# Performance work log

Hardware: AMD Instinct MI355X
Metric: run time of the kernel (lower is better)

The kernel has to match this reference:

```python
import jax, jax.numpy as jnp
import numpy as np


def _conv2d(x, w, b, stride, pad):
    out = jax.lax.conv_general_dilated(
        x, w, (stride, stride), [(pad, pad), (pad, pad)],
        dimension_numbers=('NCHW', 'OIHW', 'NCHW'))
    return out + b[None, :, None, None]


def setup_inputs() -> dict:
    key = jax.random.key(0)
    ks = jax.random.split(key, 7)
    B, C, H, W = 8, 64, 128, 128
    OC, KH, KW = 64, 3, 3
    K = KH * KW
    stdv = 1.0 / np.sqrt(C * KH * KW)
    x = jax.random.normal(ks[0], (B, C, H, W), dtype=jnp.float32)
    weight = jax.random.uniform(ks[1], (OC, C, KH, KW), minval=-stdv, maxval=stdv, dtype=jnp.float32)
    bias = jnp.zeros((OC,), dtype=jnp.float32)
    # original inits these to zero (degenerate); use small random values so the
    # learned-offset bilinear sampling path is actually exercised
    offset_w = jax.random.normal(ks[2], (2 * K, C, KH, KW), dtype=jnp.float32) * 0.01
    offset_b = jax.random.normal(ks[3], (2 * K,), dtype=jnp.float32) * 0.1
    mask_w = jax.random.normal(ks[4], (K, C, KH, KW), dtype=jnp.float32) * 0.01
    mask_b = jax.random.normal(ks[5], (K,), dtype=jnp.float32) * 0.1
    return {"x": x, "weight": weight, "bias": bias,
            "offset_w": offset_w, "offset_b": offset_b,
            "mask_w": mask_w, "mask_b": mask_b}


def _deform_conv2d(x, weight, bias, offset, mask, stride, pad):
    B, C, H, W = x.shape
    OC, _, KH, KW = weight.shape
    K = KH * KW
    Ho, Wo = offset.shape[2], offset.shape[3]
    # offset channel layout: [dy_0, dx_0, dy_1, dx_1, ...] (torchvision)
    off = offset.reshape(B, K, 2, Ho, Wo)
    dy, dx = off[:, :, 0], off[:, :, 1]            # [B,K,Ho,Wo]
    ky, kx = jnp.meshgrid(jnp.arange(KH), jnp.arange(KW), indexing='ij')
    ky = ky.reshape(1, K, 1, 1).astype(x.dtype)
    kx = kx.reshape(1, K, 1, 1).astype(x.dtype)
    gy = (jnp.arange(Ho) * stride - pad).astype(x.dtype)[None, None, :, None]
    gx = (jnp.arange(Wo) * stride - pad).astype(x.dtype)[None, None, None, :]
    py = gy + ky + dy                              # [B,K,Ho,Wo] sample rows
    px = gx + kx + dx                              # [B,K,Ho,Wo] sample cols

    y0 = jnp.floor(py); x0 = jnp.floor(px)
    fy = py - y0; fx = px - x0
    y0i = y0.astype(jnp.int32); x0i = x0.astype(jnp.int32)

    x_flat = x.reshape(B, C, H * W)
    gather = jax.vmap(lambda xf, ix: jnp.take(xf, ix, axis=1))  # -> [B,C,K,Ho,Wo]

    val = jnp.zeros((B, C, K, Ho, Wo), dtype=x.dtype)
    corners = [(y0i, x0i, (1 - fy) * (1 - fx)),
               (y0i, x0i + 1, (1 - fy) * fx),
               (y0i + 1, x0i, fy * (1 - fx)),
               (y0i + 1, x0i + 1, fy * fx)]
    for yy, xx, wt in corners:
        valid = ((yy >= 0) & (yy < H) & (xx >= 0) & (xx < W)).astype(x.dtype)
        idx = jnp.clip(yy, 0, H - 1) * W + jnp.clip(xx, 0, W - 1)
        val = val + (wt * valid)[:, None] * gather(x_flat, idx)

    sampled = val * mask[:, None]                  # modulated (DCNv2)
    w_r = weight.reshape(OC, C, K)
    out = jnp.einsum('bckhw,ock->bohw', sampled, w_r)
    return out + bias[None, :, None, None]


def reference(x, weight, bias, offset_w, offset_b, mask_w, mask_b):
    stride, pad = 1, 1
    offset = _conv2d(x, offset_w, offset_b, stride, pad)
    mask = jax.nn.sigmoid(_conv2d(x, mask_w, mask_b, stride, pad))
    return _deform_conv2d(x, weight, bias, offset, mask, stride, pad)
```

## Files before the change

kernel.cpp:

```cpp
#include <hip/hip_runtime.h>

#define HH 128
#define WW 128
#define CC 64
#define OCC 64
#define BB 8
#define NPIX (BB * HH * WW)

typedef __attribute__((ext_vector_type(4))) float f32x4;
typedef __attribute__((ext_vector_type(2))) float f32x2;
typedef __attribute__((ext_vector_type(8))) short bf16x8;
typedef __attribute__((ext_vector_type(4))) unsigned u32x4;

#define XT_OFF 0
#define W1F_OFF 16777216
#define W2F_OFF 16814080
#define WS_FULL (16814080 + 73728)

#define WROWS 4
#define WCOLS 68
#define WIN_BYTES (WROWS * WCOLS * 128)
#define WLDS_FLOATS (64 * 72)

__device__ __forceinline__ short f2bf(float f) {
    union { float f; unsigned u; } v; v.f = f;
    unsigned r = v.u + 0x7FFF + ((v.u >> 16) & 1);
    return (short)(r >> 16);
}

__device__ __forceinline__ unsigned cvtpk_bf16(float lo, float hi) {
    unsigned r;
    asm("v_cvt_pk_bf16_f32 %0, %1, %2" : "=v"(r) : "v"(lo), "v"(hi));
    return r;
}

__device__ __forceinline__ bf16x8 bilerp8(bf16x8 r00, bf16x8 r01, bf16x8 r10, bf16x8 r11,
                                          f32x4 w) {
    u32x4 u00 = __builtin_bit_cast(u32x4, r00);
    u32x4 u01 = __builtin_bit_cast(u32x4, r01);
    u32x4 u10 = __builtin_bit_cast(u32x4, r10);
    u32x4 u11 = __builtin_bit_cast(u32x4, r11);
    u32x4 res;
#pragma unroll
    for (int j = 0; j < 4; j++) {
        f32x2 a, acc;
        a[0] = __builtin_bit_cast(float, (unsigned)(u00[j] << 16));
        a[1] = __builtin_bit_cast(float, (unsigned)(u00[j] & 0xFFFF0000u));
        acc = a * w[0];
        a[0] = __builtin_bit_cast(float, (unsigned)(u01[j] << 16));
        a[1] = __builtin_bit_cast(float, (unsigned)(u01[j] & 0xFFFF0000u));
        acc += a * w[1];
        a[0] = __builtin_bit_cast(float, (unsigned)(u10[j] << 16));
        a[1] = __builtin_bit_cast(float, (unsigned)(u10[j] & 0xFFFF0000u));
        acc += a * w[2];
        a[0] = __builtin_bit_cast(float, (unsigned)(u11[j] << 16));
        a[1] = __builtin_bit_cast(float, (unsigned)(u11[j] & 0xFFFF0000u));
        acc += a * w[3];
        res[j] = cvtpk_bf16(acc[0], acc[1]);
    }
    return __builtin_bit_cast(bf16x8, res);
}

__global__ void prep_weights(const float* __restrict__ weight,
                             const float* __restrict__ offset_w,
                             const float* __restrict__ mask_w,
                             short* __restrict__ w1f, short* __restrict__ w2f) {
    int tid = blockIdx.x * 256 + threadIdx.x;
    if (tid < 2 * 18 * 64 * 8) {
        int i = tid & 7, lane = (tid >> 3) & 63, ch = (tid >> 9) % 18, tile = tid / (18 * 512);
        int r = tile * 16 + (lane & 15);
        int q = ch * 32 + ((lane >> 4) << 3) + i;
        int k = q >> 6, c = q & 63;
        float v = 0.f;
        if (r < 18)      v = offset_w[(r * CC + c) * 9 + k];
        else if (r < 27) v = mask_w[((r - 18) * CC + c) * 9 + k];
        w1f[tid] = f2bf(v);
    } else {
        int u = tid - 18432;
        if (u < 4 * 18 * 64 * 8) {
            int i = u & 7, lane = (u >> 3) & 63, ch = (u >> 9) % 18, tile = u / (18 * 512);
            int oc = tile * 16 + (lane & 15);
            int q = ch * 32 + ((lane >> 4) << 3) + i;
            int k = q >> 6, c = q & 63;
            w2f[u] = f2bf(weight[(oc * CC + c) * 9 + k]);
        }
    }
}

__global__ __launch_bounds__(256) void transpose_x(
    const float* __restrict__ x, unsigned short* __restrict__ xt) {
    __shared__ float lds[128 * 65];
    int bh = blockIdx.x;
    int b = bh >> 7, h = bh & 127;
    const float* xr = x + ((size_t)b * CC * HH + h) * WW;
    int tid = threadIdx.x;
#pragma unroll
    for (int it = 0; it < 32; it++) {
        int e = it * 256 + tid;
        int c = e >> 7, w = e & 127;
        lds[w * 65 + c] = xr[(size_t)c * HH * WW + w];
    }
    __syncthreads();
    unsigned* otr = (unsigned*)(xt + (size_t)bh * WW * CC);
#pragma unroll
    for (int it = 0; it < 16; it++) {
        int e = it * 256 + tid;
        int w = e >> 5, cp = e & 31;
        unsigned lo = (unsigned short)f2bf(lds[w * 65 + 2 * cp]);
        unsigned hi = (unsigned short)f2bf(lds[w * 65 + 2 * cp + 1]);
        otr[e] = lo | (hi << 16);
    }
}

__global__ __launch_bounds__(256) void fused_mfma(
    const unsigned short* __restrict__ xt,
    const float* __restrict__ offset_b,
    const float* __restrict__ mask_b,
    const float* __restrict__ bias,
    const short* __restrict__ w1f,
    const short* __restrict__ w2f,
    float* __restrict__ out) {
    __shared__ char shbuf[WIN_BYTES + WLDS_FLOATS * 4];
    char* win = shbuf;
    float* wlds = (float*)(shbuf + WIN_BYTES);
    float* colds = wlds;

    int lane = threadIdx.x & 63;
    int wv = threadIdx.x >> 6;
    int bid = blockIdx.x;
    int logical = (bid & 7) * 256 + (bid >> 3);
    int col = lane & 15;
    int qg = lane >> 4;
    int pl = wv * 16 + col;
    int p = logical * 64 + pl;
    int ow = p & (WW - 1);
    int oh = (p >> 7) & (HH - 1);
    int b = p >> 14;
    int ow0 = ow & ~63;
    const unsigned short* xb = xt + (size_t)b * CC * HH * WW;

    int ylo = max(0, oh - 1), yhi = min(HH - 1, oh + 2);
    int xlo = max(0, ow0 - 2), xhi = min(WW - 1, ow0 + 65);
    int R = yhi - ylo + 1, C = xhi - xlo + 1;

    {
        int C8 = C * 8;
        for (int ry = 0; ry < R; ry++) {
            const unsigned short* src = xb + ((size_t)(ylo + ry) * WW + xlo) * CC;
            for (int t = threadIdx.x; t < C8; t += 256) {
                int rx = t >> 3, s = t & 7;
                u32x4 v = *(const u32x4*)(src + rx * CC + s * 8);
                int pix = ry * WCOLS + rx;
                *(u32x4*)(win + (pix << 7) + ((s ^ (pix & 7)) << 4)) = v;
            }
        }
    }
    __syncthreads();

    {
        f32x4 acc0 = {0.f,0.f,0.f,0.f}, acc1 = {0.f,0.f,0.f,0.f};
#pragma unroll
        for (int ch = 0; ch < 18; ch++) {
            int k = ch >> 1;
            int iy = oh - 1 + k / 3;
            int ix = ow - 1 + (k - (k / 3) * 3);
            bool vv = (iy >= 0) && (iy < HH) && (ix >= 0) && (ix < WW);
            bf16x8 bfr = {0,0,0,0,0,0,0,0};
            if (vv) {
                int pix = (iy - ylo) * WCOLS + (ix - xlo);
                int s = ((ch & 1) << 2) + qg;
                bfr = *(const bf16x8*)(win + (pix << 7) + ((s ^ (pix & 7)) << 4));
            }
            bf16x8 a0 = *(const bf16x8*)(w1f + ((size_t)(0 * 18 + ch) * 64 + lane) * 8);
            bf16x8 a1 = *(const bf16x8*)(w1f + ((size_t)(1 * 18 + ch) * 64 + lane) * 8);
            acc0 = __builtin_amdgcn_mfma_f32_16x16x32_bf16(a0, bfr, acc0, 0, 0, 0);
            acc1 = __builtin_amdgcn_mfma_f32_16x16x32_bf16(a1, bfr, acc1, 0, 0, 0);
        }
#pragma unroll
        for (int j = 0; j < 4; j++) {
            int r0 = (qg << 2) + j;
            int r1 = 16 + r0;
            float b1 = (r1 < 18) ? offset_b[r1] : (r1 < 27 ? mask_b[r1 - 18] : 0.f);
            colds[pl * 33 + r0] = acc0[j] + offset_b[r0];
            colds[pl * 33 + r1] = acc1[j] + b1;
        }
    }
    __syncthreads();

    float hw[3][4];
    unsigned ho[3][4];
    {
        const float* cop = &colds[pl * 33];
#pragma unroll
        for (int ki = 0; ki < 3; ki++) {
            int k = qg + ki * 4;
            if (k < 9) {
                float dy = cop[2 * k];
                float dx = cop[2 * k + 1];
                float mr = cop[18 + k];
                float m = 1.f / (1.f + __expf(-mr));
                float py = (float)(oh - 1 + k / 3) + dy;
                float px = (float)(ow - 1 + (k - (k / 3) * 3)) + dx;
                float y0f = floorf(py), x0f = floorf(px);
                float fy = py - y0f, fx = px - x0f;
                int y0 = (int)y0f, x0 = (int)x0f;
                int y1 = y0 + 1, x1 = x0 + 1;
                bool vy0 = (y0 >= 0) && (y0 < HH), vy1 = (y1 >= 0) && (y1 < HH);
                bool vx0 = (x0 >= 0) && (x0 < WW), vx1 = (x1 >= 0) && (x1 < WW);
                hw[ki][0] = (vy0 && vx0) ? (1.f - fy) * (1.f - fx) * m : 0.f;
                hw[ki][1] = (vy0 && vx1) ? (1.f - fy) * fx * m : 0.f;
                hw[ki][2] = (vy1 && vx0) ? fy * (1.f - fx) * m : 0.f;
                hw[ki][3] = (vy1 && vx1) ? fy * fx * m : 0.f;
                int iy0 = min(max(y0, 0), HH - 1), iy1 = min(max(y1, 0), HH - 1);
                int ix0 = min(max(x0, 0), WW - 1), ix1 = min(max(x1, 0), WW - 1);
                int wy0 = iy0 - ylo, wy1 = iy1 - ylo;
                int wx0 = ix0 - xlo, wx1 = ix1 - xlo;
                bool fast = (wy0 >= 0) && (wy1 < R) && (wx0 >= 0) && (wx1 < C);
                if (fast) {
                    ho[ki][0] = (unsigned)((wy0 * WCOLS + wx0) << 7);
                    ho[ki][1] = (unsigned)((wy0 * WCOLS + wx1) << 7);
                    ho[ki][2] = (unsigned)((wy1 * WCOLS + wx0) << 7);
                    ho[ki][3] = (unsigned)((wy1 * WCOLS + wx1) << 7);
                } else {
                    ho[ki][0] = (unsigned)((iy0 * WW + ix0) * CC) | 0x80000000u;
                    ho[ki][1] = (unsigned)((iy0 * WW + ix1) * CC) | 0x80000000u;
                    ho[ki][2] = (unsigned)((iy1 * WW + ix0) * CC) | 0x80000000u;
                    ho[ki][3] = (unsigned)((iy1 * WW + ix1) * CC) | 0x80000000u;
                }
            }
        }
    }
    __syncthreads();
#pragma unroll
    for (int ki = 0; ki < 3; ki++) {
        int k = qg + ki * 4;
        if (k < 9) {
            float* q = &wlds[pl * 72 + k * 8];
            q[0] = hw[ki][0]; q[1] = hw[ki][1]; q[2] = hw[ki][2]; q[3] = hw[ki][3];
            ((unsigned*)q)[4] = ho[ki][0]; ((unsigned*)q)[5] = ho[ki][1];
            ((unsigned*)q)[6] = ho[ki][2]; ((unsigned*)q)[7] = ho[ki][3];
        }
    }
    __syncthreads();

    f32x4 acc0 = {0.f,0.f,0.f,0.f}, acc1 = {0.f,0.f,0.f,0.f};
    f32x4 acc2 = {0.f,0.f,0.f,0.f}, acc3 = {0.f,0.f,0.f,0.f};
    const float* wp = &wlds[pl * 72];
    const unsigned short* xq = xb + (qg << 3);
    unsigned sh0 = (unsigned)(qg << 4);
    unsigned sh1 = sh0 + 64;

#pragma unroll
    for (int k = 0; k < 9; k++) {
        f32x4 wq = *(const f32x4*)(wp + k * 8);
        u32x4 o = __builtin_bit_cast(u32x4, *(const f32x4*)(wp + k * 8 + 4));
        bf16x8 h0[4], h1[4];
        if (!(o[0] & 0x80000000u)) {
#pragma unroll
            for (int c = 0; c < 4; c++) {
                unsigned base = o[c];
                unsigned swz = (base >> 3) & 0x70;
                h0[c] = *(const bf16x8*)(win + base + (sh0 ^ swz));
                h1[c] = *(const bf16x8*)(win + base + (sh1 ^ swz));
            }
        } else {
#pragma unroll
            for (int c = 0; c < 4; c++) {
                unsigned off = o[c] & 0x7FFFFFFFu;
                h0[c] = *(const bf16x8*)(xq + off);
                h1[c] = *(const bf16x8*)(xq + off + 32);
            }
        }
        bf16x8 bf0 = bilerp8(h0[0], h0[1], h0[2], h0[3], wq);
        bf16x8 bf1 = bilerp8(h1[0], h1[1], h1[2], h1[3], wq);
#pragma unroll
        for (int h = 0; h < 2; h++) {
            bf16x8 bfr = h ? bf1 : bf0;
            int ch = 2 * k + h;
            const short* ap = w2f + ((size_t)ch * 64 + lane) * 8;
            bf16x8 a0 = *(const bf16x8*)(ap);
            bf16x8 a1 = *(const bf16x8*)(ap + 18 * 512);
            bf16x8 a2 = *(const bf16x8*)(ap + 36 * 512);
            bf16x8 a3 = *(const bf16x8*)(ap + 54 * 512);
            acc0 = __builtin_amdgcn_mfma_f32_16x16x32_bf16(a0, bfr, acc0, 0, 0, 0);
            acc1 = __builtin_amdgcn_mfma_f32_16x16x32_bf16(a1, bfr, acc1, 0, 0, 0);
            acc2 = __builtin_amdgcn_mfma_f32_16x16x32_bf16(a2, bfr, acc2, 0, 0, 0);
            acc3 = __builtin_amdgcn_mfma_f32_16x16x32_bf16(a3, bfr, acc3, 0, 0, 0);
        }
    }

    size_t ob = (size_t)b * OCC * HH * WW + (size_t)oh * WW + ow;
#pragma unroll
    for (int j = 0; j < 4; j++) {
        int r = (qg << 2) + j;
        out[ob + (size_t)r * HH * WW]        = acc0[j] + bias[r];
        out[ob + (size_t)(r + 16) * HH * WW] = acc1[j] + bias[r + 16];
        out[ob + (size_t)(r + 32) * HH * WW] = acc2[j] + bias[r + 32];
        out[ob + (size_t)(r + 48) * HH * WW] = acc3[j] + bias[r + 48];
    }
}

__global__ __launch_bounds__(256)
void deform_fused_fb(const float* __restrict__ x,
                     const float* __restrict__ weight,
                     const float* __restrict__ bias,
                     const float* __restrict__ offset_w,
                     const float* __restrict__ offset_b,
                     const float* __restrict__ mask_w,
                     const float* __restrict__ mask_b,
                     float* __restrict__ out) {
    int p = blockIdx.x * 256 + threadIdx.x;
    int ow = p & (WW - 1);
    int oh = (p >> 7) & (HH - 1);
    int b = p >> 14;
    const float* xb = x + (size_t)b * CC * HH * WW;

    float acc[27];
#pragma unroll
    for (int j = 0; j < 18; j++) acc[j] = offset_b[j];
#pragma unroll
    for (int j = 0; j < 9; j++) acc[18 + j] = mask_b[j];

    for (int c = 0; c < CC; c++) {
        const float* xc = xb + c * HH * WW;
        float xv[9];
#pragma unroll
        for (int t = 0; t < 9; t++) {
            int iy = oh - 1 + t / 3;
            int ix = ow - 1 + t % 3;
            bool v = (iy >= 0) && (iy < HH) && (ix >= 0) && (ix < WW);
            xv[t] = v ? xc[iy * WW + ix] : 0.f;
        }
#pragma unroll
        for (int t = 0; t < 9; t++)
#pragma unroll
            for (int j = 0; j < 27; j++) {
                float wv = (j < 18) ? offset_w[(j * CC + c) * 9 + t]
                                    : mask_w[((j - 18) * CC + c) * 9 + t];
                acc[j] += xv[t] * wv;
            }
    }

    float acc2[OCC];
#pragma unroll
    for (int o = 0; o < OCC; o++) acc2[o] = 0.f;

#pragma unroll
    for (int k = 0; k < 9; k++) {
        float dy = acc[2 * k], dx = acc[2 * k + 1];
        float m = 1.f / (1.f + __expf(-acc[18 + k]));
        float py = (float)(oh - 1 + k / 3) + dy;
        float px = (float)(ow - 1 + k % 3) + dx;
        float y0f = floorf(py), x0f = floorf(px);
        float fy = py - y0f, fx = px - x0f;
        int y0 = (int)y0f, x0 = (int)x0f;
        int y1 = y0 + 1, x1 = x0 + 1;
        bool vy0 = (y0 >= 0) && (y0 < HH), vy1 = (y1 >= 0) && (y1 < HH);
        bool vx0 = (x0 >= 0) && (x0 < WW), vx1 = (x1 >= 0) && (x1 < WW);
        float w00 = (vy0 && vx0) ? (1.f - fy) * (1.f - fx) * m : 0.f;
        float w01 = (vy0 && vx1) ? (1.f - fy) * fx * m : 0.f;
        float w10 = (vy1 && vx0) ? fy * (1.f - fx) * m : 0.f;
        float w11 = (vy1 && vx1) ? fy * fx * m : 0.f;
        int iy0 = min(max(y0, 0), HH - 1), iy1 = min(max(y1, 0), HH - 1);
        int ix0 = min(max(x0, 0), WW - 1), ix1 = min(max(x1, 0), WW - 1);
        int o00 = iy0 * WW + ix0, o01 = iy0 * WW + ix1;
        int o10 = iy1 * WW + ix0, o11 = iy1 * WW + ix1;
        for (int c = 0; c < CC; c++) {
            const float* xc = xb + c * HH * WW;
            float v = w00 * xc[o00] + w01 * xc[o01] + w10 * xc[o10] + w11 * xc[o11];
#pragma unroll
            for (int o = 0; o < OCC; o++) acc2[o] += v * weight[(o * CC + c) * 9 + k];
        }
    }
    float* ob = out + (size_t)b * OCC * HH * WW + oh * WW + ow;
#pragma unroll
    for (int o = 0; o < OCC; o++) ob[(size_t)o * HH * WW] = acc2[o] + bias[o];
}

extern "C" void kernel_launch(void* const* d_in, const int* in_sizes, int n_in,
                              void* d_out, int out_size, void* d_ws, size_t ws_size,
                              hipStream_t stream) {
    const float* x        = (const float*)d_in[0];
    const float* weight   = (const float*)d_in[1];
    const float* bias     = (const float*)d_in[2];
    const float* offset_w = (const float*)d_in[3];
    const float* offset_b = (const float*)d_in[4];
    const float* mask_w   = (const float*)d_in[5];
    const float* mask_b   = (const float*)d_in[6];
    float* out = (float*)d_out;

    if (ws_size >= (size_t)WS_FULL) {
        unsigned short* xt = (unsigned short*)((char*)d_ws + XT_OFF);
        short* w1f = (short*)((char*)d_ws + W1F_OFF);
        short* w2f = (short*)((char*)d_ws + W2F_OFF);
        prep_weights<<<216, 256, 0, stream>>>(weight, offset_w, mask_w, w1f, w2f);
        transpose_x<<<BB * HH, 256, 0, stream>>>(x, xt);
        fused_mfma<<<NPIX / 64, 256, 0, stream>>>(xt, offset_b, mask_b, bias, w1f, w2f, out);
    } else {
        deform_fused_fb<<<NPIX / 256, 256, 0, stream>>>(x, weight, bias, offset_w, offset_b,
                                                        mask_w, mask_b, out);
    }
}
```

Before: 76.71 us.

## Compute bilinear tap params per-thread in registers, drop LDS exchange buffer

Each lane now computes the bilinear weights and packed window positions for all 9 taps in registers, instead of computing 3 taps and exchanging them through a shared-memory buffer. This removes that buffer and two barriers. The sample window is narrowed to 66 columns, the offset-staging stride is shrunk, and launch bounds request 4 blocks per SIMD to raise occupancy. The cost is about 4x redundant per-tap arithmetic across lane groups, plus higher register pressure under the tighter launch bound, which could cause spills.

```diff
diff --git a/kernel.cpp b/kernel.cpp
--- a/kernel.cpp
+++ b/kernel.cpp
@@ -18,9 +18,10 @@
 #define WS_FULL (16814080 + 73728)
 
 #define WROWS 4
-#define WCOLS 68
+#define WCOLS 66
 #define WIN_BYTES (WROWS * WCOLS * 128)
-#define WLDS_FLOATS (64 * 72)
+#define CO_STRIDE 28
+#define SH_TOTAL (WIN_BYTES + 64 * CO_STRIDE * 4)
 
 __device__ __forceinline__ short f2bf(float f) {
     union { float f; unsigned u; } v; v.f = f;
@@ -112,7 +113,7 @@
     }
 }
 
-__global__ __launch_bounds__(256) void fused_mfma(
+__global__ __launch_bounds__(256, 4) void fused_mfma(
     const unsigned short* __restrict__ xt,
     const float* __restrict__ offset_b,
     const float* __restrict__ mask_b,
@@ -120,10 +121,9 @@
     const short* __restrict__ w1f,
     const short* __restrict__ w2f,
     float* __restrict__ out) {
-    __shared__ char shbuf[WIN_BYTES + WLDS_FLOATS * 4];
+    __shared__ __align__(16) char shbuf[SH_TOTAL];
     char* win = shbuf;
-    float* wlds = (float*)(shbuf + WIN_BYTES);
-    float* colds = wlds;
+    float* colds = (float*)(shbuf + WIN_BYTES);
 
     int lane = threadIdx.x & 63;
     int wv = threadIdx.x >> 6;
@@ -140,7 +140,7 @@
     const unsigned short* xb = xt + (size_t)b * CC * HH * WW;
 
     int ylo = max(0, oh - 1), yhi = min(HH - 1, oh + 2);
-    int xlo = max(0, ow0 - 2), xhi = min(WW - 1, ow0 + 65);
+    int xlo = max(0, ow0 - 1), xhi = min(WW - 1, ow0 + 64);
     int R = yhi - ylo + 1, C = xhi - xlo + 1;
 
     {
@@ -180,96 +180,94 @@
         for (int j = 0; j < 4; j++) {
             int r0 = (qg << 2) + j;
             int r1 = 16 + r0;
-            float b1 = (r1 < 18) ? offset_b[r1] : (r1 < 27 ? mask_b[r1 - 18] : 0.f);
-            colds[pl * 33 + r0] = acc0[j] + offset_b[r0];
-            colds[pl * 33 + r1] = acc1[j] + b1;
+            colds[pl * CO_STRIDE + r0] = acc0[j] + offset_b[r0];
+            if (r1 < 27) {
+                float b1 = (r1 < 18) ? offset_b[r1] : mask_b[r1 - 18];
+                colds[pl * CO_STRIDE + r1] = acc1[j] + b1;
+            }
         }
     }
     __syncthreads();
 
-    float hw[3][4];
-    unsigned ho[3][4];
+    f32x4 hwq[9];
+    unsigned hpos[9];
     {
-        const float* cop = &colds[pl * 33];
-#pragma unroll
-        for (int ki = 0; ki < 3; ki++) {
-            int k = qg + ki * 4;
-            if (k < 9) {
-                float dy = cop[2 * k];
-                float dx = cop[2 * k + 1];
-                float mr = cop[18 + k];
-                float m = 1.f / (1.f + __expf(-mr));
-                float py = (float)(oh - 1 + k / 3) + dy;
-                float px = (float)(ow - 1 + (k - (k / 3) * 3)) + dx;
-                float y0f = floorf(py), x0f = floorf(px);
-                float fy = py - y0f, fx = px - x0f;
-                int y0 = (int)y0f, x0 = (int)x0f;
-                int y1 = y0 + 1, x1 = x0 + 1;
-                bool vy0 = (y0 >= 0) && (y0 < HH), vy1 = (y1 >= 0) && (y1 < HH);
-                bool vx0 = (x0 >= 0) && (x0 < WW), vx1 = (x1 >= 0) && (x1 < WW);
-                hw[ki][0] = (vy0 && vx0) ? (1.f - fy) * (1.f - fx) * m : 0.f;
-                hw[ki][1] = (vy0 && vx1) ? (1.f - fy) * fx * m : 0.f;
-                hw[ki][2] = (vy1 && vx0) ? fy * (1.f - fx) * m : 0.f;
-                hw[ki][3] = (vy1 && vx1) ? fy * fx * m : 0.f;
-                int iy0 = min(max(y0, 0), HH - 1), iy1 = min(max(y1, 0), HH - 1);
-                int ix0 = min(max(x0, 0), WW - 1), ix1 = min(max(x1, 0), WW - 1);
-                int wy0 = iy0 - ylo, wy1 = iy1 - ylo;
-                int wx0 = ix0 - xlo, wx1 = ix1 - xlo;
-                bool fast = (wy0 >= 0) && (wy1 < R) && (wx0 >= 0) && (wx1 < C);
-                if (fast) {
-                    ho[ki][0] = (unsigned)((wy0 * WCOLS + wx0) << 7);
-                    ho[ki][1] = (unsigned)((wy0 * WCOLS + wx1) << 7);
-                    ho[ki][2] = (unsigned)((wy1 * WCOLS + wx0) << 7);
-                    ho[ki][3] = (unsigned)((wy1 * WCOLS + wx1) << 7);
-                } else {
-                    ho[ki][0] = (unsigned)((iy0 * WW + ix0) * CC) | 0x80000000u;
-                    ho[ki][1] = (unsigned)((iy0 * WW + ix1) * CC) | 0x80000000u;
-                    ho[ki][2] = (unsigned)((iy1 * WW + ix0) * CC) | 0x80000000u;
-                    ho[ki][3] = (unsigned)((iy1 * WW + ix1) * CC) | 0x80000000u;
-                }
-            }
-        }
-    }
-    __syncthreads();
-#pragma unroll
-    for (int ki = 0; ki < 3; ki++) {
-        int k = qg + ki * 4;
-        if (k < 9) {
-            float* q = &wlds[pl * 72 + k * 8];
-            q[0] = hw[ki][0]; q[1] = hw[ki][1]; q[2] = hw[ki][2]; q[3] = hw[ki][3];
-            ((unsigned*)q)[4] = ho[ki][0]; ((unsigned*)q)[5] = ho[ki][1];
-            ((unsigned*)q)[6] = ho[ki][2]; ((unsigned*)q)[7] = ho[ki][3];
-        }
-    }
-    __syncthreads();
+        const float* cop = &colds[pl * CO_STRIDE];
+#pragma unroll
+        for (int k = 0; k < 9; k++) {
+            float dy = cop[2 * k];
+            float dx = cop[2 * k + 1];
+            float mr = cop[18 + k];
+            float m = 1.f / (1.f + __expf(-mr));
+            int kd3 = k / 3;
+            float py = (float)(oh - 1 + kd3) + dy;
+            float px = (float)(ow - 1 + (k - kd3 * 3)) + dx;
+            float y0f = floorf(py), x0f = floorf(px);
+            float fy = py - y0f, fx = px - x0f;
+            int y0 = (int)y0f, x0 = (int)x0f;
+            int y1 = y0 + 1, x1 = x0 + 1;
+            bool vy0 = (y0 >= 0) && (y0 < HH), vy1 = (y1 >= 0) && (y1 < HH);
+            bool vx0 = (x0 >= 0) && (x0 < WW), vx1 = (x1 >= 0) && (x1 < WW);
+            hwq[k][0] = (vy0 && vx0) ? (1.f - fy) * (1.f - fx) * m : 0.f;
+            hwq[k][1] = (vy0 && vx1) ? (1.f - fy) * fx * m : 0.f;
+            hwq[k][2] = (vy1 && vx0) ? fy * (1.f - fx) * m : 0.f;
+            hwq[k][3] = (vy1 && vx1) ? fy * fx * m : 0.f;
+            int iy0 = min(max(y0, 0), HH - 1), iy1 = min(max(y1, 0), HH - 1);
+            int ix0 = min(max(x0, 0), WW - 1), ix1 = min(max(x1, 0), WW - 1);
+            int yinc = iy1 - iy0, xinc = ix1 - ix0;
+            int wy0 = iy0 - ylo, wx0 = ix0 - xlo;
+            bool fast = (wy0 >= 0) && (iy1 - ylo <= R - 1) &&
+                        (wx0 >= 0) && (ix1 - xlo <= C - 1);
+            hpos[k] = fast
+                ? ((unsigned)wx0 | ((unsigned)xinc << 7) | ((unsigned)wy0 << 8) |
+                   ((unsigned)yinc << 15))
+                : ((unsigned)ix0 | ((unsigned)xinc << 7) | ((unsigned)iy0 << 8) |
+                   ((unsigned)yinc << 15) | 0x10000u);
+        }
+    }
 
     f32x4 acc0 = {0.f,0.f,0.f,0.f}, acc1 = {0.f,0.f,0.f,0.f};
     f32x4 acc2 = {0.f,0.f,0.f,0.f}, acc3 = {0.f,0.f,0.f,0.f};
-    const float* wp = &wlds[pl * 72];
-    const unsigned short* xq = xb + (qg << 3);
     unsigned sh0 = (unsigned)(qg << 4);
     unsigned sh1 = sh0 + 64;
+    const char* xbb = (const char*)xb + (qg << 4);
 
 #pragma unroll
     for (int k = 0; k < 9; k++) {
-        f32x4 wq = *(const f32x4*)(wp + k * 8);
-        u32x4 o = __builtin_bit_cast(u32x4, *(const f32x4*)(wp + k * 8 + 4));
+        f32x4 wq = hwq[k];
+        unsigned pos = hpos[k];
+        unsigned x0c = pos & 127, xi = (pos >> 7) & 1;
+        unsigned y0c = (pos >> 8) & 127, yi = (pos >> 15) & 1;
         bf16x8 h0[4], h1[4];
-        if (!(o[0] & 0x80000000u)) {
-#pragma unroll
-            for (int c = 0; c < 4; c++) {
-                unsigned base = o[c];
-                unsigned swz = (base >> 3) & 0x70;
-                h0[c] = *(const bf16x8*)(win + base + (sh0 ^ swz));
-                h1[c] = *(const bf16x8*)(win + base + (sh1 ^ swz));
-            }
+        if (!(pos & 0x10000u)) {
+            unsigned p00 = y0c * WCOLS + x0c;
+            unsigned p01 = p00 + xi;
+            unsigned p10 = p00 + yi * WCOLS;
+            unsigned p11 = p10 + xi;
+            unsigned a00 = p00 << 7, a01 = p01 << 7, a10 = p10 << 7, a11 = p11 << 7;
+            unsigned s00 = (p00 & 7) << 4, s01 = (p01 & 7) << 4;
+            unsigned s10 = (p10 & 7) << 4, s11 = (p11 & 7) << 4;
+            h0[0] = *(const bf16x8*)(win + a00 + (sh0 ^ s00));
+            h0[1] = *(const bf16x8*)(win + a01 + (sh0 ^ s01));
+            h0[2] = *(const bf16x8*)(win + a10 + (sh0 ^ s10));
+            h0[3] = *(const bf16x8*)(win + a11 + (sh0 ^ s11));
+            h1[0] = *(const bf16x8*)(win + a00 + (sh1 ^ s00));
+            h1[1] = *(const bf16x8*)(win + a01 + (sh1 ^ s01));
+            h1[2] = *(const bf16x8*)(win + a10 + (sh1 ^ s10));
+            h1[3] = *(const bf16x8*)(win + a11 + (sh1 ^ s11));
         } else {
-#pragma unroll
-            for (int c = 0; c < 4; c++) {
-                unsigned off = o[c] & 0x7FFFFFFFu;
-                h0[c] = *(const bf16x8*)(xq + off);
-                h1[c] = *(const bf16x8*)(xq + off + 32);
-            }
+            unsigned g00 = (y0c * WW + x0c) << 7;
+            unsigned g01 = g00 + (xi << 7);
+            unsigned g10 = g00 + ((yi * WW) << 7);
+            unsigned g11 = g10 + (xi << 7);
+            h0[0] = *(const bf16x8*)(xbb + g00);
+            h0[1] = *(const bf16x8*)(xbb + g01);
+            h0[2] = *(const bf16x8*)(xbb + g10);
+            h0[3] = *(const bf16x8*)(xbb + g11);
+            h1[0] = *(const bf16x8*)(xbb + g00 + 64);
+            h1[1] = *(const bf16x8*)(xbb + g01 + 64);
+            h1[2] = *(const bf16x8*)(xbb + g10 + 64);
+            h1[3] = *(const bf16x8*)(xbb + g11 + 64);
         }
         bf16x8 bf0 = bilerp8(h0[0], h0[1], h0[2], h0[3], wq);
         bf16x8 bf1 = bilerp8(h1[0], h1[1], h1[2], h1[3], wq);
```

Result: slower. 95.49 us (+24.5%).
